# Kernel optimization log

Measured on AMD Instinct MI355X. Metric: run time of the kernel, lower is better.

## Reference

```python
import jax, jax.numpy as jnp
import numpy as np

N_NODES = 40000
N_EDGES = 640000
D_FEAT = 128


def setup_inputs() -> dict:
    key = jax.random.key(0)
    k1, k2, k3, k4, k5 = jax.random.split(key, 5)
    x = jax.random.normal(k1, (N_NODES, D_FEAT), dtype=jnp.float32)
    edge_rows = jax.random.randint(k2, (N_EDGES,), 0, N_NODES, dtype=jnp.int32)
    edge_cols = jax.random.randint(k3, (N_EDGES,), 0, N_NODES, dtype=jnp.int32)
    adj_vals = jax.random.uniform(k4, (N_EDGES,), dtype=jnp.float32)
    bias = jax.random.normal(k5, (D_FEAT,), dtype=jnp.float32)
    return {"x": x, "edge_rows": edge_rows, "edge_cols": edge_cols,
            "adj_vals": adj_vals, "bias": bias}


def reference(x, edge_rows, edge_cols, adj_vals, bias):
    # SpMM: out[r] = sum_e adj_vals[e] * x[edge_cols[e]] for edges with row r
    msgs = adj_vals[:, None] * x[edge_cols]                    # [E, D]
    agg = jax.ops.segment_sum(msgs, edge_rows, num_segments=N_NODES)  # [E,D]->[N,D]
    # degree = sparse row-sum of adj values
    deg = jax.ops.segment_sum(adj_vals, edge_rows, num_segments=N_NODES)  # [N]
    deg = deg[:, None]
    # mean aggregation; rows with zero degree give NaN in torch, masked to 0
    out = jnp.where(deg == 0, 0.0, agg / jnp.where(deg == 0, 1.0, deg))
    return out + bias
```

## Files before the change

kernel.cpp:

```cpp
#include <hip/hip_runtime.h>

#define N_NODES 40000
#define N_EDGES 640000
#define D_FEAT  128
#define CAP     32
#define OCAP    8192
#define NSLICE  8
#define SLICE_NODES 5000
#define STAGE_BLOCKS 625
#define BINCAP  192
#define QCAP    98304
#define CONSUME_BLOCKS 2048
#define CONV_BLOCKS 5000
#define SCAN_BLOCK 256
#define N_SCAN_BLOCKS ((N_NODES + SCAN_BLOCK - 1) / SCAN_BLOCK)

typedef float    f32x4 __attribute__((ext_vector_type(4)));

__device__ __forceinline__ unsigned bf16r(float f) {
    unsigned u = __float_as_uint(f);
    return (u + 0x7FFFu + ((u >> 16) & 1u)) >> 16;
}


__global__ __launch_bounds__(256) void stage_kernel(
    const int*   __restrict__ rows,
    const int*   __restrict__ cols,
    const float* __restrict__ vals,
    int*          __restrict__ cursors,
    unsigned*     __restrict__ bucket,
    int2*         __restrict__ overflow,
    int*          __restrict__ tails,
    uint2*        __restrict__ queue)
{
    __shared__ int cnt[NSLICE];
    __shared__ int base_g[NSLICE];
    __shared__ uint2 bin[NSLICE][BINCAP];

    if (threadIdx.x < NSLICE) cnt[threadIdx.x] = 0;
    __syncthreads();

    int vidx = blockIdx.x * 256 + threadIdx.x;
    int4   r4 = ((const int4*)  rows)[vidx];
    int4   c4 = ((const int4*)  cols)[vidx];
    float4 v4 = ((const float4*)vals)[vidx];
    int    rr[4] = { r4.x, r4.y, r4.z, r4.w };
    int    cc[4] = { c4.x, c4.y, c4.z, c4.w };
    float  vv[4] = { v4.x, v4.y, v4.z, v4.w };

    #pragma unroll
    for (int j = 0; j < 4; ++j) {
        int r = rr[j];
        unsigned p = ((unsigned)cc[j] << 16) | bf16r(vv[j]);
        int sl = r / SLICE_NODES;
        int idx = atomicAdd(&cnt[sl], 1);
        if (idx < BINCAP) {
            bin[sl][idx] = make_uint2(p, (unsigned)r);
        } else {
            int o = atomicAdd(&tails[sl], 1);
            if (o < QCAP) queue[(size_t)sl * QCAP + o] = make_uint2(p, (unsigned)r);
            else {
                int slot = atomicAdd(&cursors[r], 1);
                if (slot < CAP) bucket[(unsigned)r * CAP + slot] = p;
                else { int o2 = atomicAdd(&cursors[N_NODES], 1);
                       if (o2 < OCAP) overflow[o2] = make_int2(r, (int)p); }
            }
        }
    }
    __syncthreads();

    if (threadIdx.x < NSLICE) {
        int c = min(cnt[threadIdx.x], BINCAP);
        cnt[threadIdx.x] = c;
        base_g[threadIdx.x] = atomicAdd(&tails[threadIdx.x], c);
    }
    __syncthreads();

    #pragma unroll
    for (int s = 0; s < NSLICE; ++s) {
        int c  = cnt[s];
        int bs = base_g[s];
        for (int i = threadIdx.x; i < c; i += 256) {
            int gpos = bs + i;
            uint2 rec = bin[s][i];
            if (gpos < QCAP) {
                queue[(size_t)s * QCAP + gpos] = rec;
            } else {
                int r = (int)rec.y;
                int slot = atomicAdd(&cursors[r], 1);
                if (slot < CAP) bucket[(unsigned)r * CAP + slot] = rec.x;
                else { int o2 = atomicAdd(&cursors[N_NODES], 1);
                       if (o2 < OCAP) overflow[o2] = make_int2(r, (int)rec.x); }
            }
        }
    }
}

__global__ __launch_bounds__(256, 8) void consume_kernel(
    const float* __restrict__ x,
    const int*   __restrict__ tails,
    const uint2* __restrict__ queue,
    int*          __restrict__ cursors,
    unsigned*     __restrict__ bucket,
    int2*         __restrict__ overflow,
    uint2*        __restrict__ xbf)
{
    int b = blockIdx.x;
    if (b < CONSUME_BLOCKS) {
        int s = b & 7;
        int j = b >> 3;
        int n = min(tails[s], QCAP);
        const uint2* q = queue + (size_t)s * QCAP;
        for (int i = j * 256 + threadIdx.x; i < n; i += (CONSUME_BLOCKS / 8) * 256) {
            uint2 rec = q[i];
            int r = (int)rec.y;
            int slot = atomicAdd(&cursors[r], 1);
            if (slot < CAP) bucket[(unsigned)r * CAP + slot] = rec.x;
            else { int o = atomicAdd(&cursors[N_NODES], 1);
                   if (o < OCAP) overflow[o] = make_int2(r, (int)rec.x); }
        }
        return;
    }
    int idx = (b - CONSUME_BLOCKS) * 256 + threadIdx.x;
    float4 f = ((const float4*)x)[idx];
    uint2 o;
    o.x = bf16r(f.x) | (bf16r(f.y) << 16);
    o.y = bf16r(f.z) | (bf16r(f.w) << 16);
    xbf[idx] = o;
}

__global__ __launch_bounds__(256, 8) void gather_bf_kernel(
    const uint2*    __restrict__ xbf,
    const int*      __restrict__ cursors,
    const unsigned* __restrict__ bucket,
    const int2*     __restrict__ overflow,
    const float*    __restrict__ bias,
    float*          __restrict__ out)
{
    int b    = blockIdx.x;
    int hw   = threadIdx.x >> 5;
    int lane = threadIdx.x & 31;
    int node = (b & 7) * SLICE_NODES + (b >> 3) * 8 + hw;

    int k = min(cursors[node], CAP);
    const unsigned* base = bucket + (unsigned)node * CAP;

    unsigned ent = (lane < k) ? base[lane] : 0xFFFFFFFFu;

    #pragma unroll
    for (int kk = 2; kk <= 32; kk <<= 1) {
        #pragma unroll
        for (int j = kk >> 1; j > 0; j >>= 1) {
            unsigned other = __shfl_xor(ent, j, 64);
            bool up      = ((lane & kk) == 0);
            bool lower   = ((lane & j) == 0);
            unsigned mn  = min(ent, other), mx = max(ent, other);
            ent = (up == lower) ? mn : mx;
        }
    }

    int wb = threadIdx.x & 32;

    float4 acc0 = make_float4(0.f, 0.f, 0.f, 0.f);
    float4 acc1 = make_float4(0.f, 0.f, 0.f, 0.f);
    float  deg  = 0.f;

    #define ACC(P_, W_, A_)  {                                             \
        float _v = __uint_as_float((P_) << 16);                            \
        float _f0 = __uint_as_float((W_).x << 16);                         \
        float _f1 = __uint_as_float((W_).x & 0xFFFF0000u);                 \
        float _f2 = __uint_as_float((W_).y << 16);                         \
        float _f3 = __uint_as_float((W_).y & 0xFFFF0000u);                 \
        deg += _v;                                                         \
        A_.x += _v * _f0; A_.y += _v * _f1;                                \
        A_.z += _v * _f2; A_.w += _v * _f3; }

    #define PROC(E_, A_)  {                                                \
        unsigned _en = (E_);                                               \
        uint2 _wv = xbf[(_en >> 16) * 32u + (unsigned)lane];               \
        ACC(_en, _wv, A_); }

    int e = 0;
    for (; e + 8 <= k; e += 8) {
        unsigned p0 = __shfl(ent, wb + e,     64);
        unsigned p1 = __shfl(ent, wb + e + 1, 64);
        unsigned p2 = __shfl(ent, wb + e + 2, 64);
        unsigned p3 = __shfl(ent, wb + e + 3, 64);
        unsigned p4 = __shfl(ent, wb + e + 4, 64);
        unsigned p5 = __shfl(ent, wb + e + 5, 64);
        unsigned p6 = __shfl(ent, wb + e + 6, 64);
        unsigned p7 = __shfl(ent, wb + e + 7, 64);
        uint2 w0 = xbf[(p0 >> 16) * 32u + (unsigned)lane];
        uint2 w1 = xbf[(p1 >> 16) * 32u + (unsigned)lane];
        uint2 w2 = xbf[(p2 >> 16) * 32u + (unsigned)lane];
        uint2 w3 = xbf[(p3 >> 16) * 32u + (unsigned)lane];
        uint2 w4 = xbf[(p4 >> 16) * 32u + (unsigned)lane];
        uint2 w5 = xbf[(p5 >> 16) * 32u + (unsigned)lane];
        uint2 w6 = xbf[(p6 >> 16) * 32u + (unsigned)lane];
        uint2 w7 = xbf[(p7 >> 16) * 32u + (unsigned)lane];
        ACC(p0, w0, acc0); ACC(p1, w1, acc1);
        ACC(p2, w2, acc0); ACC(p3, w3, acc1);
        ACC(p4, w4, acc0); ACC(p5, w5, acc1);
        ACC(p6, w6, acc0); ACC(p7, w7, acc1);
    }
    for (; e + 4 <= k; e += 4) {
        unsigned p0 = __shfl(ent, wb + e,     64);
        unsigned p1 = __shfl(ent, wb + e + 1, 64);
        unsigned p2 = __shfl(ent, wb + e + 2, 64);
        unsigned p3 = __shfl(ent, wb + e + 3, 64);
        uint2 w0 = xbf[(p0 >> 16) * 32u + (unsigned)lane];
        uint2 w1 = xbf[(p1 >> 16) * 32u + (unsigned)lane];
        uint2 w2 = xbf[(p2 >> 16) * 32u + (unsigned)lane];
        uint2 w3 = xbf[(p3 >> 16) * 32u + (unsigned)lane];
        ACC(p0, w0, acc0); ACC(p1, w1, acc1);
        ACC(p2, w2, acc0); ACC(p3, w3, acc1);
    }
    for (; e < k; ++e) {
        unsigned p = __shfl(ent, wb + e, 64);
        PROC(p, acc0);
    }

    int oc = min(cursors[N_NODES], OCAP);
    for (int i = 0; i < oc; ++i) {
        int2 entv = overflow[i];
        if (entv.x == node) PROC((unsigned)entv.y, acc0);
    }
    #undef PROC
    #undef ACC

    float inv = (deg == 0.f) ? 0.f : 1.f / deg;
    float4 bv = ((const float4*)bias)[lane];
    f32x4 ov;
    ov.x = (acc0.x + acc1.x) * inv + bv.x;
    ov.y = (acc0.y + acc1.y) * inv + bv.y;
    ov.z = (acc0.z + acc1.z) * inv + bv.z;
    ov.w = (acc0.w + acc1.w) * inv + bv.w;
    __builtin_nontemporal_store(ov, (f32x4*)(out + (size_t)node * D_FEAT) + lane);
}


__global__ __launch_bounds__(256) void histogram_kernel(
    const int* __restrict__ rows, int* __restrict__ counts)
{
    int e = blockIdx.x * blockDim.x + threadIdx.x;
    if (e < N_EDGES) atomicAdd(&counts[rows[e]], 1);
}

__global__ __launch_bounds__(SCAN_BLOCK) void scan1_kernel(
    const int* __restrict__ counts, int* __restrict__ offsets, int* __restrict__ blocksums)
{
    __shared__ int tmp[SCAN_BLOCK];
    int t = threadIdx.x;
    int g = blockIdx.x * SCAN_BLOCK + t;
    int v = (g < N_NODES) ? counts[g] : 0;
    tmp[t] = v;
    __syncthreads();
    #pragma unroll
    for (int off = 1; off < SCAN_BLOCK; off <<= 1) {
        int add = (t >= off) ? tmp[t - off] : 0;
        __syncthreads();
        tmp[t] += add;
        __syncthreads();
    }
    if (g < N_NODES) offsets[g] = tmp[t] - v;
    if (t == SCAN_BLOCK - 1) blocksums[blockIdx.x] = tmp[t];
}

__global__ __launch_bounds__(SCAN_BLOCK) void scan2_kernel(int* __restrict__ blocksums)
{
    __shared__ int tmp[SCAN_BLOCK];
    int t = threadIdx.x;
    int v = (t < N_SCAN_BLOCKS) ? blocksums[t] : 0;
    tmp[t] = v;
    __syncthreads();
    #pragma unroll
    for (int off = 1; off < SCAN_BLOCK; off <<= 1) {
        int add = (t >= off) ? tmp[t - off] : 0;
        __syncthreads();
        tmp[t] += add;
        __syncthreads();
    }
    if (t < N_SCAN_BLOCKS) blocksums[t] = tmp[t] - v;
}

__global__ __launch_bounds__(SCAN_BLOCK) void scan3_kernel(
    int* __restrict__ offsets, int* __restrict__ cursors, const int* __restrict__ blocksums)
{
    int t = threadIdx.x;
    int g = blockIdx.x * SCAN_BLOCK + t;
    if (g < N_NODES) {
        int o = offsets[g] + blocksums[blockIdx.x];
        offsets[g] = o;
        cursors[g] = o;
    }
    if (g == 0) offsets[N_NODES] = N_EDGES;
}

__global__ __launch_bounds__(256) void bucket_kernel(
    const int* __restrict__ rows, const int* __restrict__ cols,
    const float* __restrict__ vals, int* __restrict__ cursors, int2* __restrict__ bucket)
{
    int e = blockIdx.x * blockDim.x + threadIdx.x;
    if (e >= N_EDGES) return;
    int r = rows[e];
    int pos = atomicAdd(&cursors[r], 1);
    bucket[pos] = make_int2(cols[e], __float_as_int(vals[e]));
}

__global__ __launch_bounds__(256) void gather_csr_kernel(
    const float* __restrict__ x, const int* __restrict__ offsets,
    const int2* __restrict__ bucket, const float* __restrict__ bias,
    float* __restrict__ out)
{
    int t = blockIdx.x * blockDim.x + threadIdx.x;
    int node = t >> 5;
    if (node >= N_NODES) return;
    int lane = t & 31;
    int beg = offsets[node];
    int end = offsets[node + 1];
    float4 acc = make_float4(0.f, 0.f, 0.f, 0.f);
    float deg = 0.f;
    int2 ent = (beg < end) ? bucket[beg] : make_int2(0, 0);
    for (int e = beg; e < end; ++e) {
        int2 cur = ent;
        if (e + 1 < end) ent = bucket[e + 1];
        float v = __int_as_float(cur.y);
        deg += v;
        float4 xv = ((const float4*)(x + (size_t)cur.x * D_FEAT))[lane];
        acc.x += v * xv.x; acc.y += v * xv.y; acc.z += v * xv.z; acc.w += v * xv.w;
    }
    float inv = (deg == 0.f) ? 0.f : 1.f / deg;
    float4 bv = ((const float4*)bias)[lane];
    float4 ov;
    ov.x = acc.x * inv + bv.x; ov.y = acc.y * inv + bv.y;
    ov.z = acc.z * inv + bv.z; ov.w = acc.w * inv + bv.w;
    ((float4*)(out + (size_t)node * D_FEAT))[lane] = ov;
}


__global__ __launch_bounds__(256) void edge_scatter_kernel(
    const float* __restrict__ x, const int* __restrict__ rows,
    const int* __restrict__ cols, const float* __restrict__ vals,
    float* __restrict__ agg, float* __restrict__ deg)
{
    int t = blockIdx.x * blockDim.x + threadIdx.x;
    int edge = t >> 5;
    if (edge >= N_EDGES) return;
    int lane = t & 31;
    int row = rows[edge]; int col = cols[edge]; float v = vals[edge];
    float4 xv = ((const float4*)(x + (size_t)col * D_FEAT))[lane];
    float* dst = agg + (size_t)row * D_FEAT + lane * 4;
    unsafeAtomicAdd(dst + 0, v * xv.x);
    unsafeAtomicAdd(dst + 1, v * xv.y);
    unsafeAtomicAdd(dst + 2, v * xv.z);
    unsafeAtomicAdd(dst + 3, v * xv.w);
    if (lane == 0) unsafeAtomicAdd(deg + row, v);
}

__global__ __launch_bounds__(256) void finalize_kernel(
    float* __restrict__ out, const float* __restrict__ deg, const float* __restrict__ bias)
{
    int t = blockIdx.x * blockDim.x + threadIdx.x;
    int node = t >> 5;
    if (node >= N_NODES) return;
    int lane = t & 31;
    float d = deg[node];
    float inv = (d == 0.f) ? 0.f : 1.f / d;
    float4* o = (float4*)(out + (size_t)node * D_FEAT) + lane;
    float4 bv = ((const float4*)bias)[lane];
    float4 ov = *o;
    ov.x = ov.x * inv + bv.x; ov.y = ov.y * inv + bv.y;
    ov.z = ov.z * inv + bv.z; ov.w = ov.w * inv + bv.w;
    *o = ov;
}


extern "C" void kernel_launch(void* const* d_in, const int* in_sizes, int n_in,
                              void* d_out, int out_size, void* d_ws, size_t ws_size,
                              hipStream_t stream) {
    const float* x    = (const float*)d_in[0];
    const int*   rows = (const int*)  d_in[1];
    const int*   cols = (const int*)  d_in[2];
    const float* vals = (const float*)d_in[3];
    const float* bias = (const float*)d_in[4];
    float* out = (float*)d_out;

    char* wb = (char*)d_ws;
    int*      f_cursors  = (int*)     wb;
    int*      f_tails    = (int*)    (wb + 160032);
    int2*     f_overflow = (int2*)   (wb + 160128);
    uint2*    f_xbf      = (uint2*)  (wb + 225792);
    unsigned* f_bucket   = (unsigned*)(wb + 10465792);
    uint2*    f_queue    = (uint2*)  (wb + 15585792);
    size_t need_fast = 15585792 + (size_t)NSLICE * QCAP * 8;

    int* w = (int*)d_ws;
    size_t need_csr = ((size_t)120448 + 2u * N_EDGES) * sizeof(int);

    if (ws_size >= need_fast) {
        (void)hipMemsetAsync(f_cursors, 0, 160064, stream);
        stage_kernel<<<STAGE_BLOCKS, 256, 0, stream>>>(
            rows, cols, vals, f_cursors, f_bucket, f_overflow, f_tails, f_queue);
        consume_kernel<<<CONSUME_BLOCKS + CONV_BLOCKS, 256, 0, stream>>>(
            x, f_tails, f_queue, f_cursors, f_bucket, f_overflow, f_xbf);
        gather_bf_kernel<<<N_NODES / 8, 256, 0, stream>>>(
            f_xbf, f_cursors, f_bucket, f_overflow, bias, out);
    } else if (ws_size >= need_csr) {
        int*  counts    = w;
        int*  offsets   = w + 40064;
        int*  cursors   = w + 80128;
        int*  blocksums = w + 120128;
        int2* bucket    = (int2*)(w + 120448);
        (void)hipMemsetAsync(counts, 0, N_NODES * sizeof(int), stream);
        histogram_kernel<<<(N_EDGES + 255) / 256, 256, 0, stream>>>(rows, counts);
        scan1_kernel<<<N_SCAN_BLOCKS, SCAN_BLOCK, 0, stream>>>(counts, offsets, blocksums);
        scan2_kernel<<<1, SCAN_BLOCK, 0, stream>>>(blocksums);
        scan3_kernel<<<N_SCAN_BLOCKS, SCAN_BLOCK, 0, stream>>>(offsets, cursors, blocksums);
        bucket_kernel<<<(N_EDGES + 255) / 256, 256, 0, stream>>>(rows, cols, vals, cursors, bucket);
        int threads = N_NODES * 32;
        gather_csr_kernel<<<(threads + 255) / 256, 256, 0, stream>>>(x, offsets, bucket, bias, out);
    } else {
        float* deg = (float*)d_ws;
        (void)hipMemsetAsync(out, 0, (size_t)N_NODES * D_FEAT * sizeof(float), stream);
        (void)hipMemsetAsync(deg, 0, (size_t)N_NODES * sizeof(float), stream);
        int et = N_EDGES * 32;
        edge_scatter_kernel<<<(et + 255) / 256, 256, 0, stream>>>(x, rows, cols, vals, out, deg);
        int nt = N_NODES * 32;
        finalize_kernel<<<(nt + 255) / 256, 256, 0, stream>>>(out, deg, bias);
    }
}
```

Baseline: 142.0 us.

## Build per-node edge buckets in shared memory per node range in consume kernel

```diff
diff --git a/kernel.cpp b/kernel.cpp
--- a/kernel.cpp
+++ b/kernel.cpp
@@ -10,7 +10,9 @@
 #define STAGE_BLOCKS 625
 #define BINCAP  192
 #define QCAP    98304
-#define CONSUME_BLOCKS 2048
+#define CBLK_PER_SLICE 32
+#define CONSUME_BLOCKS (NSLICE * CBLK_PER_SLICE)
+#define RANGE_MAX 157
 #define CONV_BLOCKS 5000
 #define SCAN_BLOCK 256
 #define N_SCAN_BLOCKS ((N_NODES + SCAN_BLOCK - 1) / SCAN_BLOCK)
@@ -96,7 +98,7 @@
     }
 }
 
-__global__ __launch_bounds__(256, 8) void consume_kernel(
+__global__ __launch_bounds__(256) void consume_kernel(
     const float* __restrict__ x,
     const int*   __restrict__ tails,
     const uint2* __restrict__ queue,
@@ -109,16 +111,37 @@
     if (b < CONSUME_BLOCKS) {
         int s = b & 7;
         int j = b >> 3;
+        int loc0  = (j * SLICE_NODES) / CBLK_PER_SLICE;
+        int loc1  = ((j + 1) * SLICE_NODES) / CBLK_PER_SLICE;
+        int range = loc1 - loc0;
+        int node0 = s * SLICE_NODES + loc0;
+
+        __shared__ int      lcnt[RANGE_MAX];
+        __shared__ unsigned lbuck[RANGE_MAX][CAP];
+
+        for (int i = threadIdx.x; i < range; i += 256) lcnt[i] = 0;
+        __syncthreads();
+
         int n = min(tails[s], QCAP);
         const uint2* q = queue + (size_t)s * QCAP;
-        for (int i = j * 256 + threadIdx.x; i < n; i += (CONSUME_BLOCKS / 8) * 256) {
+        for (int i = threadIdx.x; i < n; i += 256) {
             uint2 rec = q[i];
-            int r = (int)rec.y;
-            int slot = atomicAdd(&cursors[r], 1);
-            if (slot < CAP) bucket[(unsigned)r * CAP + slot] = rec.x;
-            else { int o = atomicAdd(&cursors[N_NODES], 1);
-                   if (o < OCAP) overflow[o] = make_int2(r, (int)rec.x); }
+            unsigned ln = rec.y - (unsigned)node0;
+            if (ln < (unsigned)range) {
+                int idx = atomicAdd(&lcnt[ln], 1);
+                if (idx < CAP) lbuck[ln][idx] = rec.x;
+                else { int o = atomicAdd(&cursors[N_NODES], 1);
+                       if (o < OCAP) overflow[o] = make_int2((int)rec.y, (int)rec.x); }
+            }
         }
+        __syncthreads();
+
+        for (int i = threadIdx.x; i < range; i += 256)
+            cursors[node0 + i] = lcnt[i];
+        const unsigned* lb = &lbuck[0][0];
+        unsigned* gb = bucket + (size_t)node0 * CAP;
+        for (int w = threadIdx.x; w < range * CAP; w += 256)
+            gb[w] = lb[w];
         return;
     }
     int idx = (b - CONSUME_BLOCKS) * 256 + threadIdx.x;
```

New measurement: 205.7 us. 44.8% more time.
